# Performance work log

Hardware: AMD Instinct MI355X
Metric: run time of the kernel (lower is better)

## Reference

```python
import jax, jax.numpy as jnp
import numpy as np

N, IN, OUT = 4096, 256, 256


def setup_inputs() -> dict:
    key = jax.random.key(0)
    k = jax.random.split(key, 7)
    return {
        "x": jax.random.normal(k[0], (N, IN), dtype=jnp.float32),
        "eps_w": jax.random.normal(k[1], (N, IN, OUT), dtype=jnp.float32),
        "eps_b": jax.random.normal(k[2], (N, OUT), dtype=jnp.float32),
        # learned parameters (init ranges per the torch module)
        "w_param1": jax.random.uniform(k[3], (IN, OUT), minval=-0.01, maxval=0.01, dtype=jnp.float32),
        "logw_param2": jax.random.uniform(k[4], (IN, OUT), minval=-4.0, maxval=-2.0, dtype=jnp.float32),
        "b_param1": jax.random.uniform(k[5], (OUT,), minval=-0.01, maxval=0.01, dtype=jnp.float32),
        "logb_param2": jax.random.uniform(k[6], (OUT,), minval=-4.0, maxval=-2.0, dtype=jnp.float32),
    }


def reference(x, eps_w, eps_b, w_param1, logw_param2, b_param1, logb_param2):
    # Per-sample reparameterized Gaussian weights: Normal(mu, exp(log_sigma)).sample((N,))
    weights = w_param1[None] + jnp.exp(logw_param2)[None] * eps_w   # [N, IN, OUT]
    biases = b_param1[None] + jnp.exp(logb_param2)[None] * eps_b    # [N, OUT]
    # (x.unsqueeze(1) @ weights).squeeze(1) + biases  ->  batched matvec
    return jnp.einsum("ni,nio->no", x, weights) + biases
```

## Files before the change

kernel.cpp:

```cpp
#include <hip/hip_runtime.h>

#define N_ROWS  4096
#define IN_DIM  256
#define OUT_DIM 256

#define TA 1024
#define RA 16
#define TB 1024
#define RB 16

typedef float f32x4 __attribute__((ext_vector_type(4)));

__device__ __forceinline__ float4 nt_load4(const float4* p) {
    f32x4 v = __builtin_nontemporal_load((const f32x4*)p);
    return make_float4(v.x, v.y, v.z, v.w);
}

__device__ __forceinline__ unsigned short f32_to_bf16(float f) {
    unsigned u = __float_as_uint(f);
    u += 0x7FFFu + ((u >> 16) & 1u);
    return (unsigned short)(u >> 16);
}
__device__ __forceinline__ float bf16_to_f32(unsigned short h) {
    return __uint_as_float(((unsigned)h) << 16);
}

__global__ void bayes_exp_kernel(const float* __restrict__ logw,
                                 unsigned short* __restrict__ swb) {
    int idx = blockIdx.x * blockDim.x + threadIdx.x;
    if (idx < IN_DIM * OUT_DIM) swb[idx] = f32_to_bf16(__expf(logw[idx]));
}

__global__ __launch_bounds__(TA) void bayes_base_kernel(
    const float* __restrict__ x,
    const float* __restrict__ eps_b,
    const float* __restrict__ w1,
    const float* __restrict__ b1,
    const float* __restrict__ logb2,
    float* __restrict__ out)
{
    __shared__ float xs[RA * IN_DIM];
    const int tid = threadIdx.x;
    const int n0  = blockIdx.x * RA;

    ((float4*)xs)[tid] = ((const float4*)(x + (size_t)n0 * IN_DIM))[tid];
    __syncthreads();

    const int row = tid >> 6;
    const int o4  = tid & 63;
    const int n   = n0 + row;

    const float4* w4 = (const float4*)w1 + o4;
    float4 acc = make_float4(0.f, 0.f, 0.f, 0.f);

    #pragma unroll 4
    for (int i = 0; i < IN_DIM; ++i) {
        const float  xv = xs[row * IN_DIM + i];
        const float4 w  = w4[i * (OUT_DIM / 4)];
        acc.x = fmaf(xv, w.x, acc.x);
        acc.y = fmaf(xv, w.y, acc.y);
        acc.z = fmaf(xv, w.z, acc.z);
        acc.w = fmaf(xv, w.w, acc.w);
    }

    const float4 eb = nt_load4((const float4*)(eps_b + (size_t)n * OUT_DIM) + o4);
    const float4 b  = ((const float4*)b1)[o4];
    const float4 lb = ((const float4*)logb2)[o4];

    float4 res;
    res.x = acc.x + fmaf(__expf(lb.x), eb.x, b.x);
    res.y = acc.y + fmaf(__expf(lb.y), eb.y, b.y);
    res.z = acc.z + fmaf(__expf(lb.z), eb.z, b.z);
    res.w = acc.w + fmaf(__expf(lb.w), eb.w, b.w);

    ((float4*)(out + (size_t)n * OUT_DIM))[o4] = res;
}

template <bool PRE>
__global__ __launch_bounds__(TB) void bayes_eps_kernel(
    const float* __restrict__ x,
    const float* __restrict__ eps_w,
    const void*  __restrict__ swsrc,
    float* __restrict__ out)
{
    __shared__ uint4 swbuf[IN_DIM * OUT_DIM / 8];
    __shared__ float xs[RB * IN_DIM];

    const int tid = threadIdx.x;
    const int n0  = blockIdx.x * RB;

    if (PRE) {
        const uint4* src = (const uint4*)swsrc;
        #pragma unroll
        for (int r = 0; r < 8; ++r)
            swbuf[tid + r * TB] = src[tid + r * TB];
    } else {
        const float4* src = (const float4*)swsrc;
        unsigned short* dst = (unsigned short*)swbuf;
        #pragma unroll
        for (int r = 0; r < 16; ++r) {
            const int   j = tid + r * TB;
            const float4 v = src[j];
            ushort4 h;
            h.x = f32_to_bf16(__expf(v.x));
            h.y = f32_to_bf16(__expf(v.y));
            h.z = f32_to_bf16(__expf(v.z));
            h.w = f32_to_bf16(__expf(v.w));
            *(ushort4*)(dst + j * 4) = h;
        }
    }
    ((float4*)xs)[tid] = ((const float4*)(x + (size_t)n0 * IN_DIM))[tid];
    __syncthreads();

    const int row = tid >> 6;
    const int o4  = tid & 63;
    const int n   = n0 + row;

    const unsigned short* swp = (const unsigned short*)swbuf;
    const float4* e4 = (const float4*)(eps_w + (size_t)n * IN_DIM * OUT_DIM) + o4;

    float4 acc = make_float4(0.f, 0.f, 0.f, 0.f);

    #pragma unroll 8
    for (int i = 0; i < IN_DIM; ++i) {
        const float   xv = xs[row * IN_DIM + i];
        const ushort4 h  = *(const ushort4*)(swp + i * OUT_DIM + o4 * 4);
        const float4  e  = nt_load4(e4 + i * (OUT_DIM / 4));
        acc.x = fmaf(xv * bf16_to_f32(h.x), e.x, acc.x);
        acc.y = fmaf(xv * bf16_to_f32(h.y), e.y, acc.y);
        acc.z = fmaf(xv * bf16_to_f32(h.z), e.z, acc.z);
        acc.w = fmaf(xv * bf16_to_f32(h.w), e.w, acc.w);
    }

    float4* op = (float4*)(out + (size_t)n * OUT_DIM) + o4;
    float4 base = *op;
    base.x += acc.x;
    base.y += acc.y;
    base.z += acc.z;
    base.w += acc.w;
    *op = base;
}

extern "C" void kernel_launch(void* const* d_in, const int* in_sizes, int n_in,
                              void* d_out, int out_size, void* d_ws, size_t ws_size,
                              hipStream_t stream) {
    const float* x     = (const float*)d_in[0];
    const float* eps_w = (const float*)d_in[1];
    const float* eps_b = (const float*)d_in[2];
    const float* w1    = (const float*)d_in[3];
    const float* logw2 = (const float*)d_in[4];
    const float* b1    = (const float*)d_in[5];
    const float* logb2 = (const float*)d_in[6];
    float* out = (float*)d_out;

    const size_t need = (size_t)(IN_DIM * OUT_DIM) * sizeof(unsigned short);

    bayes_base_kernel<<<N_ROWS / RA, TA, 0, stream>>>(
        x, eps_b, w1, b1, logb2, out);

    if (ws_size >= need) {
        unsigned short* swb = (unsigned short*)d_ws;
        bayes_exp_kernel<<<(IN_DIM * OUT_DIM + 1023) / 1024, 1024, 0, stream>>>(
            logw2, swb);
        bayes_eps_kernel<true><<<N_ROWS / RB, TB, 0, stream>>>(
            x, eps_w, swb, out);
    } else {
        bayes_eps_kernel<false><<<N_ROWS / RB, TB, 0, stream>>>(
            x, eps_w, logw2, out);
    }
}
```

Baseline: 210.9 us.

## Fuse base matvec, exp precompute, and eps matvec into one kernel

Merges the three launches (mean-weight matvec with bias, exp/bf16 precompute of sigma, and the eps_w streaming matvec) into one kernel. Each block now computes exp(logw) into shared memory itself, accumulates x@w1 alongside the eps term, and writes the output once. This removes two kernel launches and the read-modify-write of out. In exchange every block repeats the exp conversion from fp32 logw and adds w1 loads inside the bandwidth-bound eps loop.

Result: faster. 176.0 us (-16.5%).

```diff
diff --git a/kernel.cpp b/kernel.cpp
--- a/kernel.cpp
+++ b/kernel.cpp
@@ -4,10 +4,8 @@
 #define IN_DIM  256
 #define OUT_DIM 256
 
-#define TA 1024
-#define RA 16
-#define TB 1024
-#define RB 16
+#define TB  1024
+#define RB  16
 
 typedef float f32x4 __attribute__((ext_vector_type(4)));
 
@@ -25,62 +23,14 @@
     return __uint_as_float(((unsigned)h) << 16);
 }
 
-__global__ void bayes_exp_kernel(const float* __restrict__ logw,
-                                 unsigned short* __restrict__ swb) {
-    int idx = blockIdx.x * blockDim.x + threadIdx.x;
-    if (idx < IN_DIM * OUT_DIM) swb[idx] = f32_to_bf16(__expf(logw[idx]));
-}
-
-__global__ __launch_bounds__(TA) void bayes_base_kernel(
+__global__ __launch_bounds__(TB) void bayes_fused_kernel(
     const float* __restrict__ x,
+    const float* __restrict__ eps_w,
     const float* __restrict__ eps_b,
     const float* __restrict__ w1,
+    const float* __restrict__ logw2,
     const float* __restrict__ b1,
     const float* __restrict__ logb2,
-    float* __restrict__ out)
-{
-    __shared__ float xs[RA * IN_DIM];
-    const int tid = threadIdx.x;
-    const int n0  = blockIdx.x * RA;
-
-    ((float4*)xs)[tid] = ((const float4*)(x + (size_t)n0 * IN_DIM))[tid];
-    __syncthreads();
-
-    const int row = tid >> 6;
-    const int o4  = tid & 63;
-    const int n   = n0 + row;
-
-    const float4* w4 = (const float4*)w1 + o4;
-    float4 acc = make_float4(0.f, 0.f, 0.f, 0.f);
-
-    #pragma unroll 4
-    for (int i = 0; i < IN_DIM; ++i) {
-        const float  xv = xs[row * IN_DIM + i];
-        const float4 w  = w4[i * (OUT_DIM / 4)];
-        acc.x = fmaf(xv, w.x, acc.x);
-        acc.y = fmaf(xv, w.y, acc.y);
-        acc.z = fmaf(xv, w.z, acc.z);
-        acc.w = fmaf(xv, w.w, acc.w);
-    }
-
-    const float4 eb = nt_load4((const float4*)(eps_b + (size_t)n * OUT_DIM) + o4);
-    const float4 b  = ((const float4*)b1)[o4];
-    const float4 lb = ((const float4*)logb2)[o4];
-
-    float4 res;
-    res.x = acc.x + fmaf(__expf(lb.x), eb.x, b.x);
-    res.y = acc.y + fmaf(__expf(lb.y), eb.y, b.y);
-    res.z = acc.z + fmaf(__expf(lb.z), eb.z, b.z);
-    res.w = acc.w + fmaf(__expf(lb.w), eb.w, b.w);
-
-    ((float4*)(out + (size_t)n * OUT_DIM))[o4] = res;
-}
-
-template <bool PRE>
-__global__ __launch_bounds__(TB) void bayes_eps_kernel(
-    const float* __restrict__ x,
-    const float* __restrict__ eps_w,
-    const void*  __restrict__ swsrc,
     float* __restrict__ out)
 {
     __shared__ uint4 swbuf[IN_DIM * OUT_DIM / 8];
@@ -89,24 +39,19 @@
     const int tid = threadIdx.x;
     const int n0  = blockIdx.x * RB;
 
-    if (PRE) {
-        const uint4* src = (const uint4*)swsrc;
-        #pragma unroll
-        for (int r = 0; r < 8; ++r)
-            swbuf[tid + r * TB] = src[tid + r * TB];
-    } else {
-        const float4* src = (const float4*)swsrc;
+    {
+        const float4* src = (const float4*)logw2;
         unsigned short* dst = (unsigned short*)swbuf;
         #pragma unroll
         for (int r = 0; r < 16; ++r) {
-            const int   j = tid + r * TB;
+            const int    j = tid + r * TB;
             const float4 v = src[j];
             ushort4 h;
             h.x = f32_to_bf16(__expf(v.x));
             h.y = f32_to_bf16(__expf(v.y));
             h.z = f32_to_bf16(__expf(v.z));
             h.w = f32_to_bf16(__expf(v.w));
-            *(ushort4*)(dst + j * 4) = h;
+            *(ushort4*)(dst + (size_t)j * 4) = h;
         }
     }
     ((float4*)xs)[tid] = ((const float4*)(x + (size_t)n0 * IN_DIM))[tid];
@@ -118,27 +63,38 @@
 
     const unsigned short* swp = (const unsigned short*)swbuf;
     const float4* e4 = (const float4*)(eps_w + (size_t)n * IN_DIM * OUT_DIM) + o4;
+    const float4* w4 = (const float4*)w1 + o4;
 
-    float4 acc = make_float4(0.f, 0.f, 0.f, 0.f);
+    float4 acc  = make_float4(0.f, 0.f, 0.f, 0.f);
+    float4 accw = make_float4(0.f, 0.f, 0.f, 0.f);
 
     #pragma unroll 8
     for (int i = 0; i < IN_DIM; ++i) {
         const float   xv = xs[row * IN_DIM + i];
         const ushort4 h  = *(const ushort4*)(swp + i * OUT_DIM + o4 * 4);
         const float4  e  = nt_load4(e4 + i * (OUT_DIM / 4));
-        acc.x = fmaf(xv * bf16_to_f32(h.x), e.x, acc.x);
-        acc.y = fmaf(xv * bf16_to_f32(h.y), e.y, acc.y);
-        acc.z = fmaf(xv * bf16_to_f32(h.z), e.z, acc.z);
-        acc.w = fmaf(xv * bf16_to_f32(h.w), e.w, acc.w);
+        const float4  w  = w4[i * (OUT_DIM / 4)];
+        acc.x  = fmaf(xv * bf16_to_f32(h.x), e.x, acc.x);
+        acc.y  = fmaf(xv * bf16_to_f32(h.y), e.y, acc.y);
+        acc.z  = fmaf(xv * bf16_to_f32(h.z), e.z, acc.z);
+        acc.w  = fmaf(xv * bf16_to_f32(h.w), e.w, acc.w);
+        accw.x = fmaf(xv, w.x, accw.x);
+        accw.y = fmaf(xv, w.y, accw.y);
+        accw.z = fmaf(xv, w.z, accw.z);
+        accw.w = fmaf(xv, w.w, accw.w);
     }
 
-    float4* op = (float4*)(out + (size_t)n * OUT_DIM) + o4;
-    float4 base = *op;
-    base.x += acc.x;
-    base.y += acc.y;
-    base.z += acc.z;
-    base.w += acc.w;
-    *op = base;
+    const float4 eb = nt_load4((const float4*)(eps_b + (size_t)n * OUT_DIM) + o4);
+    const float4 b  = ((const float4*)b1)[o4];
+    const float4 lb = ((const float4*)logb2)[o4];
+
+    float4 res;
+    res.x = acc.x + accw.x + fmaf(__expf(lb.x), eb.x, b.x);
+    res.y = acc.y + accw.y + fmaf(__expf(lb.y), eb.y, b.y);
+    res.z = acc.z + accw.z + fmaf(__expf(lb.z), eb.z, b.z);
+    res.w = acc.w + accw.w + fmaf(__expf(lb.w), eb.w, b.w);
+
+    ((float4*)(out + (size_t)n * OUT_DIM))[o4] = res;
 }
 
 extern "C" void kernel_launch(void* const* d_in, const int* in_sizes, int n_in,
@@ -153,19 +109,6 @@
     const float* logb2 = (const float*)d_in[6];
     float* out = (float*)d_out;
 
-    const size_t need = (size_t)(IN_DIM * OUT_DIM) * sizeof(unsigned short);
-
-    bayes_base_kernel<<<N_ROWS / RA, TA, 0, stream>>>(
-        x, eps_b, w1, b1, logb2, out);
-
-    if (ws_size >= need) {
-        unsigned short* swb = (unsigned short*)d_ws;
-        bayes_exp_kernel<<<(IN_DIM * OUT_DIM + 1023) / 1024, 1024, 0, stream>>>(
-            logw2, swb);
-        bayes_eps_kernel<true><<<N_ROWS / RB, TB, 0, stream>>>(
-            x, eps_w, swb, out);
-    } else {
-        bayes_eps_kernel<false><<<N_ROWS / RB, TB, 0, stream>>>(
-            x, eps_w, logw2, out);
-    }
+    bayes_fused_kernel<<<N_ROWS / RB, TB, 0, stream>>>(
+        x, eps_w, eps_b, w1, logw2, b1, logb2, out);
 }
```
